# Kernel tuning notes

Measured on AMD Instinct MI355X. Metric: run time of the kernel, lower is better.

## Reference

```python
import jax, jax.numpy as jnp
import numpy as np
from jax import lax

K = 9          # box kernel side
PAD = K // 2   # same padding
K_SUM = float(K * K * K)


def _box_sum(x):
    """Sliding-window sum over a 9x9x9 box, zero-padded (separable 1D convs).
    x: [B, 1, D, H, W] -> same shape."""
    dn = ('NCDHW', 'OIDHW', 'NCDHW')
    for ax in range(3):  # D, H, W
        kshape = [1, 1, 1, 1, 1]
        kshape[2 + ax] = K
        w = jnp.ones(kshape, dtype=x.dtype)
        pad = [(0, 0), (0, 0), (0, 0)]
        pad[ax] = (PAD, PAD)
        x = lax.conv_general_dilated(x, w, window_strides=(1, 1, 1),
                                     padding=pad, dimension_numbers=dn)
    return x


def setup_inputs() -> dict:
    key = jax.random.key(0)
    k1, k2 = jax.random.split(key)
    shape = (2, 1, 192, 192, 192)  # [B, 1, D, H, W]
    I = jax.random.uniform(k1, shape, dtype=jnp.float32)
    J = jax.random.uniform(k2, shape, dtype=jnp.float32)
    return {"I": I, "J": J}


def reference(I, J):
    II = I * I
    JJ = J * J
    IJ = I * J
    I_sum = _box_sum(I)
    J_sum = _box_sum(J)
    II_sum = _box_sum(II)
    JJ_sum = _box_sum(JJ)
    IJ_sum = _box_sum(IJ)
    I_u = I / K_SUM
    J_u = J / K_SUM
    cross = IJ_sum - I_sum * J_u - J_sum * I_u + I_u * J_u * K_SUM
    I_var = II_sum - 2 * I_sum * I_u + I_u * I_u * K_SUM
    J_var = JJ_sum - 2 * J_sum * J_u + J_u * J_u * K_SUM
    top = cross * cross
    bottom = I_var * J_var + 1e-5
    return -jnp.mean(top / bottom)
```

## Files before the change

kernel.cpp:

```cpp
#include <hip/hip_runtime.h>
#include <hip/hip_bf16.h>

#define WDIM 192
#define PLANE (192 * 192)
#define VOL (192 * 192 * 192)
#define HC 16
#define TR (HC + 8)
#define NCH 12
#define RWU 100
#define DC 24

typedef __fp16 h2f __attribute__((ext_vector_type(2)));

__global__ void zero_out_k(float* out) { out[0] = 0.0f; }

static __device__ inline unsigned int pk_h16(float a, float b) {
    h2f v = __builtin_amdgcn_cvt_pkrtz(a, b);
    return __builtin_bit_cast(unsigned int, v);
}
static __device__ inline float dot2u(unsigned int a, unsigned int b, float c) {
    return __builtin_amdgcn_fdot2(__builtin_bit_cast(h2f, a),
                                  __builtin_bit_cast(h2f, b), c, false);
}

static __device__ inline unsigned int pk_bf16(float a, float b) {
    union { __hip_bfloat162 v; unsigned int u; } cvt;
    cvt.v = __float22bfloat162_rn(make_float2(a, b));
    return cvt.u;
}
static __device__ inline float bf_lo(unsigned int u) {
    union { unsigned int u; float f; } c; c.u = u << 16; return c.f;
}
static __device__ inline float bf_hi(unsigned int u) {
    union { unsigned int u; float f; } c; c.u = u & 0xffff0000u; return c.f;
}

__global__ __launch_bounds__(192) void wh_pass(const float* __restrict__ I,
                                               const float* __restrict__ J,
                                               unsigned int* __restrict__ B) {
    __shared__ unsigned int sI[TR * RWU];
    __shared__ unsigned int sJ[TR * RWU];
    const int t = threadIdx.x;
    const int d = blockIdx.x / NCH;
    const int c = blockIdx.x - d * NCH;
    const int h0 = c * HC;

    const size_t bofs = (size_t)blockIdx.y * VOL;
    const float* Ib = I + bofs;
    const float* Jb = J + bofs;
    unsigned int* Bb = B + bofs * 3;

    const size_t dbase = (size_t)d * PLANE;

    {
        const int row = t >> 3;
        const int p = t & 7;
        unsigned int* dst = (p < 4) ? sI : sJ;
        const int q = p & 3;
        const int col = (q < 2) ? q : (96 + q);
        dst[row * RWU + col] = 0u;
    }

    #pragma unroll
    for (int i = 0; i < 6; ++i) {
        const int idx4 = i * 192 + t;
        const int row  = idx4 / 48;
        const int col4 = (idx4 - row * 48) * 4;
        const int h = h0 - 4 + row;
        float4 vI = make_float4(0.f, 0.f, 0.f, 0.f);
        float4 vJ = vI;
        if (h >= 0 && h < WDIM) {
            vI = *(const float4*)(Ib + dbase + (size_t)h * WDIM + col4);
            vJ = *(const float4*)(Jb + dbase + (size_t)h * WDIM + col4);
        }
        uint2 uI, uJ;
        uI.x = pk_h16(vI.x, vI.y); uI.y = pk_h16(vI.z, vI.w);
        uJ.x = pk_h16(vJ.x, vJ.y); uJ.y = pk_h16(vJ.z, vJ.w);
        const int ui = row * RWU + 2 + (col4 >> 1);
        *(uint2*)&sI[ui] = uI;
        *(uint2*)&sJ[ui] = uJ;
    }
    __syncthreads();

    const int tb = t >> 1;
    const int odd = t & 1;
    const unsigned int ONESF = 0x3C003C00u;
    const unsigned int ones0 = odd ? 0x3C000000u : ONESF;
    const unsigned int ones4 = odd ? ONESF : 0x00003C00u;
    const unsigned int keep0 = odd ? 0xFFFF0000u : 0xFFFFFFFFu;
    const unsigned int keep4 = odd ? 0xFFFFFFFFu : 0x0000FFFFu;

    float ring0[9], ring1[9], ring2[9], ring3[9], ring4[9];
    #pragma unroll
    for (int j = 0; j < 9; ++j) { ring0[j]=0.f; ring1[j]=0.f; ring2[j]=0.f; ring3[j]=0.f; ring4[j]=0.f; }
    float s0 = 0.f, s1 = 0.f, s2 = 0.f, s3 = 0.f, s4 = 0.f;

    unsigned int AI[5], AJ[5], BI[5], BJ[5];
    #pragma unroll
    for (int p = 0; p < 5; ++p) { AI[p] = sI[tb + p]; AJ[p] = sJ[tb + p]; }

    #pragma unroll
    for (int s = 0; s < TR; ++s) {
        if (s + 1 < TR) {
            const int base = (s + 1) * RWU + tb;
            if ((s & 1) == 0) {
                #pragma unroll
                for (int p = 0; p < 5; ++p) { BI[p] = sI[base + p]; BJ[p] = sJ[base + p]; }
            } else {
                #pragma unroll
                for (int p = 0; p < 5; ++p) { AI[p] = sI[base + p]; AJ[p] = sJ[base + p]; }
            }
        }
        const unsigned int c0 = ((s & 1) == 0) ? AI[0] : BI[0];
        const unsigned int c1 = ((s & 1) == 0) ? AI[1] : BI[1];
        const unsigned int c2 = ((s & 1) == 0) ? AI[2] : BI[2];
        const unsigned int c3 = ((s & 1) == 0) ? AI[3] : BI[3];
        const unsigned int c4 = ((s & 1) == 0) ? AI[4] : BI[4];
        const unsigned int e0 = ((s & 1) == 0) ? AJ[0] : BJ[0];
        const unsigned int e1 = ((s & 1) == 0) ? AJ[1] : BJ[1];
        const unsigned int e2 = ((s & 1) == 0) ? AJ[2] : BJ[2];
        const unsigned int e3 = ((s & 1) == 0) ? AJ[3] : BJ[3];
        const unsigned int e4 = ((s & 1) == 0) ? AJ[4] : BJ[4];

        const unsigned int mI0 = c0 & keep0, mI4 = c4 & keep4;
        const unsigned int mJ0 = e0 & keep0, mJ4 = e4 & keep4;

        float w0 = dot2u(c0, ones0, 0.f);
        w0 = dot2u(c1, ONESF, w0); w0 = dot2u(c2, ONESF, w0);
        w0 = dot2u(c3, ONESF, w0); w0 = dot2u(c4, ones4, w0);

        float w1 = dot2u(e0, ones0, 0.f);
        w1 = dot2u(e1, ONESF, w1); w1 = dot2u(e2, ONESF, w1);
        w1 = dot2u(e3, ONESF, w1); w1 = dot2u(e4, ones4, w1);

        float w2 = dot2u(mI0, c0, 0.f);
        w2 = dot2u(c1, c1, w2); w2 = dot2u(c2, c2, w2);
        w2 = dot2u(c3, c3, w2); w2 = dot2u(mI4, c4, w2);

        float w3 = dot2u(mJ0, e0, 0.f);
        w3 = dot2u(e1, e1, w3); w3 = dot2u(e2, e2, w3);
        w3 = dot2u(e3, e3, w3); w3 = dot2u(mJ4, e4, w3);

        float w4 = dot2u(mI0, e0, 0.f);
        w4 = dot2u(c1, e1, w4); w4 = dot2u(c2, e2, w4);
        w4 = dot2u(c3, e3, w4); w4 = dot2u(mI4, e4, w4);

        const int j = s % 9;
        s0 += w0 - ring0[j]; ring0[j] = w0;
        s1 += w1 - ring1[j]; ring1[j] = w1;
        s2 += w2 - ring2[j]; ring2[j] = w2;
        s3 += w3 - ring3[j]; ring3[j] = w3;
        s4 += w4 - ring4[j]; ring4[j] = w4;

        if (s >= 8) {
            const int h_out = h0 + s - 8;
            const size_t idx = dbase + (size_t)h_out * WDIM + t;
            uint3 q;
            q.x = pk_bf16(s0, s1);
            q.y = pk_bf16(s2, s3);
            q.z = pk_bf16(s4, 0.f);
            *(uint3*)(Bb + idx * 3) = q;
        }
    }
}

__global__ __launch_bounds__(192) void d_pass(const unsigned int* __restrict__ B,
                                              const float* __restrict__ I,
                                              const float* __restrict__ J,
                                              float* __restrict__ out) {
    const int t = threadIdx.x;
    const int h = blockIdx.x >> 3;
    const int c = blockIdx.x & 7;
    const int d0 = c * DC;
    const int base_h = h * WDIM + t;

    const size_t bofs = (size_t)blockIdx.y * VOL;
    const float* Ib = I + bofs;
    const float* Jb = J + bofs;
    const unsigned int* Bb = B + bofs * 3;

    float r0[9], r1[9], r2[9], r3[9], r4[9];
    #pragma unroll
    for (int j = 0; j < 9; ++j) { r0[j]=0.f; r1[j]=0.f; r2[j]=0.f; r3[j]=0.f; r4[j]=0.f; }
    float s0 = 0.f, s1 = 0.f, s2 = 0.f, s3 = 0.f, s4 = 0.f;

    const float inv_k = 1.0f / 729.0f;
    float local = 0.f;

    uint3 qA[8], qB[8];
    float2 cA[8], cB[8];
    #pragma unroll
    for (int i = 0; i < 8; ++i) {
        const int d_in = d0 - 4 + i;
        qA[i] = make_uint3(0u, 0u, 0u);
        if (d_in >= 0 && d_in < WDIM)
            qA[i] = *(const uint3*)(Bb + ((size_t)d_in * PLANE + base_h) * 3);
        cA[i] = make_float2(0.f, 0.f);
    }

    #pragma unroll
    for (int g = 0; g < 4; ++g) {
        if (g + 1 < 4) {
            #pragma unroll
            for (int i = 0; i < 8; ++i) {
                const int s = (g + 1) * 8 + i;
                const int d_in = d0 - 4 + s;
                uint3 v = make_uint3(0u, 0u, 0u);
                if (d_in >= 0 && d_in < WDIM)
                    v = *(const uint3*)(Bb + ((size_t)d_in * PLANE + base_h) * 3);
                const int d_out = d0 + s - 8;
                const size_t cidx = (size_t)d_out * PLANE + base_h;
                const float ci = Ib[cidx];
                const float cj = Jb[cidx];
                if ((g & 1) == 0) { qB[i] = v; cB[i] = make_float2(ci, cj); }
                else              { qA[i] = v; cA[i] = make_float2(ci, cj); }
            }
        }
        #pragma unroll
        for (int i = 0; i < 8; ++i) {
            const int s = g * 8 + i;
            const uint3 q = ((g & 1) == 0) ? qA[i] : qB[i];
            const float f0 = bf_lo(q.x), f1 = bf_hi(q.x);
            const float f2 = bf_lo(q.y), f3 = bf_hi(q.y);
            const float f4 = bf_lo(q.z);
            const int j = s % 9;
            s0 += f0 - r0[j]; r0[j] = f0;
            s1 += f1 - r1[j]; r1[j] = f1;
            s2 += f2 - r2[j]; r2[j] = f2;
            s3 += f3 - r3[j]; r3[j] = f3;
            s4 += f4 - r4[j]; r4[j] = f4;

            if (s >= 8) {
                const float2 cc = ((g & 1) == 0) ? cA[i] : cB[i];
                const float Iu = cc.x * inv_k;
                const float Ju = cc.y * inv_k;
                const float cross = s4 - s0 * Ju - s1 * Iu + Iu * Ju * 729.0f;
                const float Ivar  = s2 - 2.0f * s0 * Iu + Iu * Iu * 729.0f;
                const float Jvar  = s3 - 2.0f * s1 * Ju + Ju * Ju * 729.0f;
                local += (cross * cross) / (Ivar * Jvar + 1e-5f);
            }
        }
    }

    __shared__ float sred[192];
    sred[t] = local;
    __syncthreads();
    if (t < 64) {
        float v = sred[t] + sred[t + 64] + sred[t + 128];
        #pragma unroll
        for (int off = 32; off; off >>= 1) v += __shfl_down(v, off);
        if (t == 0) {
            atomicAdd(out, v * (-1.0f / 14155776.0f));
        }
    }
}

extern "C" void kernel_launch(void* const* d_in, const int* in_sizes, int n_in,
                              void* d_out, int out_size, void* d_ws, size_t ws_size,
                              hipStream_t stream) {
    const float* I = (const float*)d_in[0];
    const float* J = (const float*)d_in[1];
    float* out = (float*)d_out;
    unsigned int* B = (unsigned int*)d_ws;

    zero_out_k<<<1, 1, 0, stream>>>(out);

    const size_t need2 = (size_t)2 * VOL * 12;
    if (ws_size >= need2) {
        wh_pass<<<dim3(192 * NCH, 2), 192, 0, stream>>>(I, J, B);
        d_pass <<<dim3(1536, 2), 192, 0, stream>>>(B, I, J, out);
    } else {
        for (int b = 0; b < 2; ++b) {
            const float* Ib = I + (size_t)b * VOL;
            const float* Jb = J + (size_t)b * VOL;
            wh_pass<<<dim3(192 * NCH, 1), 192, 0, stream>>>(Ib, Jb, B);
            d_pass <<<dim3(1536, 1), 192, 0, stream>>>(B, Ib, Jb, out);
        }
    }
}
```

Measured before the change: 233.5 us.

## Fold output zeroing into wh_pass and slim d_pass register footprint

Removes the separate zero-output launch by having the first wh_pass block clear the accumulator. In d_pass, the sliding-window ring buffer now holds packed bf16 words instead of unpacked floats, and the prefetch depth drops from groups of 8 to groups of 4; both cut register pressure to allow higher occupancy. The centre-value loads for the first 8 steps are skipped, and the final division becomes a hardware reciprocal. Risks are shallower latency hiding from the smaller prefetch and slightly lower precision from the reciprocal approximation.

Result: no change. 232.0 us (-0.6%).

```diff
diff --git a/kernel.cpp b/kernel.cpp
--- a/kernel.cpp
+++ b/kernel.cpp
@@ -12,8 +12,6 @@
 
 typedef __fp16 h2f __attribute__((ext_vector_type(2)));
 
-__global__ void zero_out_k(float* out) { out[0] = 0.0f; }
-
 static __device__ inline unsigned int pk_h16(float a, float b) {
     h2f v = __builtin_amdgcn_cvt_pkrtz(a, b);
     return __builtin_bit_cast(unsigned int, v);
@@ -37,13 +35,16 @@
 
 __global__ __launch_bounds__(192) void wh_pass(const float* __restrict__ I,
                                                const float* __restrict__ J,
-                                               unsigned int* __restrict__ B) {
+                                               unsigned int* __restrict__ B,
+                                               float* __restrict__ out0) {
     __shared__ unsigned int sI[TR * RWU];
     __shared__ unsigned int sJ[TR * RWU];
     const int t = threadIdx.x;
     const int d = blockIdx.x / NCH;
     const int c = blockIdx.x - d * NCH;
     const int h0 = c * HC;
+
+    if (out0 && blockIdx.x == 0 && blockIdx.y == 0 && t == 0) *out0 = 0.0f;
 
     const size_t bofs = (size_t)blockIdx.y * VOL;
     const float* Ib = I + bofs;
@@ -179,18 +180,18 @@
     const float* Jb = J + bofs;
     const unsigned int* Bb = B + bofs * 3;
 
-    float r0[9], r1[9], r2[9], r3[9], r4[9];
-    #pragma unroll
-    for (int j = 0; j < 9; ++j) { r0[j]=0.f; r1[j]=0.f; r2[j]=0.f; r3[j]=0.f; r4[j]=0.f; }
+    uint3 rr[9];
+    #pragma unroll
+    for (int j = 0; j < 9; ++j) rr[j] = make_uint3(0u, 0u, 0u);
     float s0 = 0.f, s1 = 0.f, s2 = 0.f, s3 = 0.f, s4 = 0.f;
 
     const float inv_k = 1.0f / 729.0f;
     float local = 0.f;
 
-    uint3 qA[8], qB[8];
-    float2 cA[8], cB[8];
-    #pragma unroll
-    for (int i = 0; i < 8; ++i) {
+    uint3 qA[4], qB[4];
+    float2 cA[4], cB[4];
+    #pragma unroll
+    for (int i = 0; i < 4; ++i) {
         const int d_in = d0 - 4 + i;
         qA[i] = make_uint3(0u, 0u, 0u);
         if (d_in >= 0 && d_in < WDIM)
@@ -199,36 +200,37 @@
     }
 
     #pragma unroll
-    for (int g = 0; g < 4; ++g) {
-        if (g + 1 < 4) {
+    for (int g = 0; g < 8; ++g) {
+        if (g + 1 < 8) {
             #pragma unroll
-            for (int i = 0; i < 8; ++i) {
-                const int s = (g + 1) * 8 + i;
+            for (int i = 0; i < 4; ++i) {
+                const int s = (g + 1) * 4 + i;
                 const int d_in = d0 - 4 + s;
                 uint3 v = make_uint3(0u, 0u, 0u);
-                if (d_in >= 0 && d_in < WDIM)
+                if (d_in < WDIM)
                     v = *(const uint3*)(Bb + ((size_t)d_in * PLANE + base_h) * 3);
-                const int d_out = d0 + s - 8;
-                const size_t cidx = (size_t)d_out * PLANE + base_h;
-                const float ci = Ib[cidx];
-                const float cj = Jb[cidx];
-                if ((g & 1) == 0) { qB[i] = v; cB[i] = make_float2(ci, cj); }
-                else              { qA[i] = v; cA[i] = make_float2(ci, cj); }
+                float2 cc = make_float2(0.f, 0.f);
+                if (s >= 8) {
+                    const int d_out = d0 + s - 8;
+                    const size_t cidx = (size_t)d_out * PLANE + base_h;
+                    cc = make_float2(Ib[cidx], Jb[cidx]);
+                }
+                if ((g & 1) == 0) { qB[i] = v; cB[i] = cc; }
+                else              { qA[i] = v; cA[i] = cc; }
             }
         }
         #pragma unroll
-        for (int i = 0; i < 8; ++i) {
-            const int s = g * 8 + i;
+        for (int i = 0; i < 4; ++i) {
+            const int s = g * 4 + i;
             const uint3 q = ((g & 1) == 0) ? qA[i] : qB[i];
-            const float f0 = bf_lo(q.x), f1 = bf_hi(q.x);
-            const float f2 = bf_lo(q.y), f3 = bf_hi(q.y);
-            const float f4 = bf_lo(q.z);
             const int j = s % 9;
-            s0 += f0 - r0[j]; r0[j] = f0;
-            s1 += f1 - r1[j]; r1[j] = f1;
-            s2 += f2 - r2[j]; r2[j] = f2;
-            s3 += f3 - r3[j]; r3[j] = f3;
-            s4 += f4 - r4[j]; r4[j] = f4;
+            const uint3 o = rr[j];
+            s0 += bf_lo(q.x) - bf_lo(o.x);
+            s1 += bf_hi(q.x) - bf_hi(o.x);
+            s2 += bf_lo(q.y) - bf_lo(o.y);
+            s3 += bf_hi(q.y) - bf_hi(o.y);
+            s4 += bf_lo(q.z) - bf_lo(o.z);
+            rr[j] = q;
 
             if (s >= 8) {
                 const float2 cc = ((g & 1) == 0) ? cA[i] : cB[i];
@@ -237,7 +239,7 @@
                 const float cross = s4 - s0 * Ju - s1 * Iu + Iu * Ju * 729.0f;
                 const float Ivar  = s2 - 2.0f * s0 * Iu + Iu * Iu * 729.0f;
                 const float Jvar  = s3 - 2.0f * s1 * Ju + Ju * Ju * 729.0f;
-                local += (cross * cross) / (Ivar * Jvar + 1e-5f);
+                local += (cross * cross) * __builtin_amdgcn_rcpf(Ivar * Jvar + 1e-5f);
             }
         }
     }
@@ -263,17 +265,16 @@
     float* out = (float*)d_out;
     unsigned int* B = (unsigned int*)d_ws;
 
-    zero_out_k<<<1, 1, 0, stream>>>(out);
-
     const size_t need2 = (size_t)2 * VOL * 12;
     if (ws_size >= need2) {
-        wh_pass<<<dim3(192 * NCH, 2), 192, 0, stream>>>(I, J, B);
+        wh_pass<<<dim3(WDIM * NCH, 2), 192, 0, stream>>>(I, J, B, out);
         d_pass <<<dim3(1536, 2), 192, 0, stream>>>(B, I, J, out);
     } else {
         for (int b = 0; b < 2; ++b) {
             const float* Ib = I + (size_t)b * VOL;
             const float* Jb = J + (size_t)b * VOL;
-            wh_pass<<<dim3(192 * NCH, 1), 192, 0, stream>>>(Ib, Jb, B);
+            wh_pass<<<dim3(WDIM * NCH, 1), 192, 0, stream>>>(Ib, Jb, B,
+                                                             b == 0 ? out : nullptr);
             d_pass <<<dim3(1536, 1), 192, 0, stream>>>(B, Ib, Jb, out);
         }
     }
```
